# Performance work log

Measured on AMD Instinct MI355X. Metric: run time of the kernel, lower is better.

Reference implementation:

```python
import jax, jax.numpy as jnp
import numpy as np

B, C, H, W, S = 32, 512, 32, 32, 4
HW = H * W
OUT = HW // S  # conv1/conv2 out channels = 256
EPS = 1e-5


def setup_inputs() -> dict:
    key = jax.random.key(0)
    ks = jax.random.split(key, 8)
    d = {}
    d["x"] = jax.random.normal(ks[0], (B, C, H, W), jnp.float32)
    # conv1 / bn1 (operate on x_flat with 'channels' = h*w)
    d["w1"] = jax.random.normal(ks[1], (OUT, HW), jnp.float32) * 0.02
    d["b1"] = jnp.zeros((OUT,), jnp.float32)
    d["g1"] = jnp.ones((OUT,), jnp.float32)
    d["be1"] = jnp.zeros((OUT,), jnp.float32)
    d["m1"] = jax.random.normal(ks[2], (OUT,), jnp.float32) * 0.01
    d["v1"] = jnp.ones((OUT,), jnp.float32)
    # conv2 / bn2
    d["w2"] = jax.random.normal(ks[3], (OUT, HW), jnp.float32) * 0.02
    d["b2"] = jnp.zeros((OUT,), jnp.float32)
    d["g2"] = jnp.ones((OUT,), jnp.float32)
    d["be2"] = jnp.zeros((OUT,), jnp.float32)
    d["m2"] = jax.random.normal(ks[4], (OUT,), jnp.float32) * 0.01
    d["v2"] = jnp.ones((OUT,), jnp.float32)
    # conv3 / bn3 (1x1 conv on the real channel dim c)
    d["w3"] = jax.random.normal(ks[5], (C, C), jnp.float32) * 0.02
    d["b3"] = jnp.zeros((C,), jnp.float32)
    d["g3"] = jnp.ones((C,), jnp.float32)
    d["be3"] = jnp.zeros((C,), jnp.float32)
    d["m3"] = jax.random.normal(ks[6], (C,), jnp.float32) * 0.01
    d["v3"] = jnp.ones((C,), jnp.float32)
    # conv4: 1x1 conv mapping 1+2c channels -> 1
    d["w4"] = jax.random.normal(ks[7], (1 + 2 * C,), jnp.float32) * 0.02
    d["b4"] = jnp.zeros((), jnp.float32)
    return d


def _bn1d(t, g, be, m, v):
    # t: [b, o, c]; BatchNorm (eval mode) over channel axis 1
    scale = g / jnp.sqrt(v + EPS)
    return (t - m[:, None]) * scale[:, None] + be[:, None]


def reference(x, w1, b1, g1, be1, m1, v1,
              w2, b2, g2, be2, m2, v2,
              w3, b3, g3, be3, m3, v3,
              w4, b4):
    b, c, h, w = x.shape
    # x_flat: [b, h*w, c] -- conv1/conv2 are 1x1 convs over 'channels' = h*w
    xf = x.reshape(b, c, h * w).transpose(0, 2, 1)
    theta = jax.nn.relu(_bn1d(jnp.einsum('oq,bqc->boc', w1, xf) + b1[:, None],
                              g1, be1, m1, v1))  # [b, OUT, c]
    phi = jax.nn.relu(_bn1d(jnp.einsum('oq,bqc->boc', w2, xf) + b2[:, None],
                            g2, be2, m2, v2))    # [b, OUT, c]
    # per-batch conv2d-as-matmul loop collapses to one batched GEMM:
    # affinity[b, i, j] = sum_k phi[b, k, i] * theta[b, k, j]
    aff = jnp.einsum('bki,bkj->bij', phi, theta)  # [b, c, c]
    # x_embed: 1x1 conv + BN + ReLU + global average pool -> [b, c]
    scale3 = g3 / jnp.sqrt(v3 + EPS)
    xe = jnp.einsum('oc,bchw->bohw', w3, x) + b3[:, None, None]
    xe = jax.nn.relu((xe - m3[:, None, None]) * scale3[:, None, None]
                     + be3[:, None, None])
    xe = xe.mean(axis=(2, 3))  # [b, c]
    # conv4 over y = cat([x_embed, affinity_a, affinity_b], dim=1):
    # affinity_a[b,i,0,p] = aff[b,i,p]; affinity_b[b,i,0,p] = aff[b,p,i]
    logits = (w4[0] * xe
              + jnp.einsum('i,bip->bp', w4[1:1 + c], aff)
              + jnp.einsum('i,bpi->bp', w4[1 + c:], aff)
              + b4)
    a = jax.nn.sigmoid(logits)  # [b, c]
    return x * a[:, :, None, None]
```

## Files before the change

kernel.cpp:

```cpp
#include <hip/hip_runtime.h>
#include <math.h>

#define BB   32
#define CC   512
#define HWW  1024
#define OUTC 256
#define EPSV 1e-5f

typedef __attribute__((ext_vector_type(8))) short bfrag;
typedef __attribute__((ext_vector_type(4))) float f32x4;

__device__ inline unsigned short f2bf(float x){
  unsigned int uu = __float_as_uint(x);
  uu += 0x7fff + ((uu >> 16) & 1);
  return (unsigned short)(uu >> 16);
}
__device__ inline float bf2f(unsigned short h){
  return __uint_as_float(((unsigned int)h) << 16);
}

#define ASYNC16(g, l) \
  __builtin_amdgcn_global_load_lds((const __attribute__((address_space(1))) unsigned int*)(g), \
                                   (__attribute__((address_space(3))) unsigned int*)(l), 16, 0, 0)

#define WAITV(N) asm volatile("s_waitcnt vmcnt(" #N ")" ::: "memory")


__global__ __launch_bounds__(256) void prep(
    const float* __restrict__ x,
    const float* __restrict__ w1, const float* __restrict__ w2,
    const float* __restrict__ w3,
    unsigned short* __restrict__ Xhi, unsigned short* __restrict__ Xlo,
    unsigned short* __restrict__ XThi,
    unsigned short* __restrict__ Whi, unsigned short* __restrict__ Wlo,
    unsigned short* __restrict__ W3hi,
    float* __restrict__ accz)
{
  if (blockIdx.z == 32) {
    int worker = (blockIdx.y * 16 + blockIdx.x) * 256 + threadIdx.x;
    accz[worker] = 0.f;
    for (int i = worker; i < 786432; i += 32768) {
      if (i < 524288) {
        float v = (i < 262144) ? w1[i] : w2[i - 262144];
        unsigned short h = f2bf(v);
        Whi[i] = h;
        Wlo[i] = f2bf(v - bf2f(h));
      } else {
        int j = i - 524288;
        W3hi[j] = f2bf(w3[j]);
      }
    }
    return;
  }
  __shared__ float T[64][65];
  const int b = blockIdx.z, c0 = blockIdx.y * 64, p0 = blockIdx.x * 64;
  const int tid = threadIdx.x, tr = tid >> 4, tc4 = (tid & 15) * 4;
  const float* xb = x + (size_t)b * 512 * 1024;
#pragma unroll
  for (int r = 0; r < 4; ++r) {
    int c = c0 + tr + r * 16;
    float4 v = *(const float4*)(xb + (size_t)c * 1024 + p0 + tc4);
    T[tr + r * 16][tc4 + 0] = v.x; T[tr + r * 16][tc4 + 1] = v.y;
    T[tr + r * 16][tc4 + 2] = v.z; T[tr + r * 16][tc4 + 3] = v.w;
    ushort4 h, l;
    h.x = f2bf(v.x); l.x = f2bf(v.x - bf2f(h.x));
    h.y = f2bf(v.y); l.y = f2bf(v.y - bf2f(h.y));
    h.z = f2bf(v.z); l.z = f2bf(v.z - bf2f(h.z));
    h.w = f2bf(v.w); l.w = f2bf(v.w - bf2f(h.w));
    size_t idx = (size_t)b * 524288 + (size_t)c * 1024 + p0 + tc4;
    *(ushort4*)(Xhi + idx) = h;
    *(ushort4*)(Xlo + idx) = l;
  }
  __syncthreads();
#pragma unroll
  for (int r = 0; r < 4; ++r) {
    int pl = tr + r * 16;
    ushort4 h;
    h.x = f2bf(T[tc4 + 0][pl]); h.y = f2bf(T[tc4 + 1][pl]);
    h.z = f2bf(T[tc4 + 2][pl]); h.w = f2bf(T[tc4 + 3][pl]);
    *(ushort4*)(XThi + (size_t)b * 524288 + (size_t)(p0 + pl) * 512 + c0 + tc4) = h;
  }
}

__global__ __launch_bounds__(256) void gemm_fused(
    const unsigned short* __restrict__ Xhi, const unsigned short* __restrict__ Xlo,
    const unsigned short* __restrict__ Whi, const unsigned short* __restrict__ Wlo,
    const unsigned short* __restrict__ W3hi, const unsigned short* __restrict__ XThi,
    const float* __restrict__ b1p, const float* __restrict__ g1p,
    const float* __restrict__ be1p, const float* __restrict__ m1p, const float* __restrict__ v1p,
    const float* __restrict__ b2p, const float* __restrict__ g2p,
    const float* __restrict__ be2p, const float* __restrict__ m2p, const float* __restrict__ v2p,
    const float* __restrict__ b3p, const float* __restrict__ g3p,
    const float* __restrict__ be3p, const float* __restrict__ m3p, const float* __restrict__ v3p,
    const float* __restrict__ w4,
    float* __restrict__ P2, float* __restrict__ u, float* __restrict__ t,
    float* __restrict__ xe_acc)
{
  __shared__ unsigned short smem[24576];
  const int fid  = blockIdx.x;
  const int tid  = threadIdx.x;
  const int wave = tid >> 6, lane = tid & 63;
  const int lr = lane >> 2;
  const int lcs = ((lane & 3) ^ (lr & 3)) * 8;
  const int fr = lane & 15, fq = lane >> 4;
  const int fsw = (fq ^ (fr & 3)) * 8;

  if (fid < 1024) {
    const int xcd = fid & 7;
    const int n0  = ((fid >> 3) & 7) * 64;
    const int bc  = ((fid >> 6) << 3) | xcd;
    const int b   = bc >> 2;
    const int c0  = (bc & 3) * 128;
    const int wm = wave & 1, wn = wave >> 1;

    const unsigned short* gb; int lboff; int ninst;
    if (wave == 0)      { gb = Xhi + (size_t)b * 524288 + (size_t)c0 * 1024; lboff = 0;     ninst = 8; }
    else if (wave == 1) { gb = Xlo + (size_t)b * 524288 + (size_t)c0 * 1024; lboff = 4096;  ninst = 8; }
    else if (wave == 2) { gb = Whi + (size_t)n0 * 1024; lboff = 8192;  ninst = 4; }
    else                { gb = Wlo + (size_t)n0 * 1024; lboff = 10240; ninst = 4; }
    gb += (size_t)lr * 1024 + lcs;

    f32x4 acc[4][2];
    const f32x4 zz = {0.f, 0.f, 0.f, 0.f};
#pragma unroll
    for (int i = 0; i < 4; ++i) { acc[i][0] = zz; acc[i][1] = zz; }

    for (int inst = 0; inst < ninst; ++inst)
      ASYNC16(gb + (size_t)inst * 16 * 1024, smem + lboff + inst * 512);

    int cur = 0;
    for (int kq = 0; kq < 1024; kq += 32) {
      __builtin_amdgcn_sched_barrier(0);
      if (kq + 32 < 1024) {
        unsigned short* nb = smem + (cur ^ 1) * 12288 + lboff;
        for (int inst = 0; inst < ninst; ++inst)
          ASYNC16(gb + (size_t)inst * 16 * 1024 + kq + 32, nb + inst * 512);
        if (wave < 2) WAITV(8); else WAITV(4);
      } else {
        WAITV(0);
      }
      __builtin_amdgcn_s_barrier();
      __builtin_amdgcn_sched_barrier(0);

      const unsigned short* bufc = smem + cur * 12288;
      const unsigned short* sAh = bufc;
      const unsigned short* sAl = bufc + 4096;
      const unsigned short* sBh = bufc + 8192;
      const unsigned short* sBl = bufc + 10240;
      bfrag ah[4], al[4], bh[2], bl[2];
#pragma unroll
      for (int i = 0; i < 4; ++i) {
        int off = (wm * 64 + i * 16 + fr) * 32 + fsw;
        ah[i] = *(const bfrag*)&sAh[off];
        al[i] = *(const bfrag*)&sAl[off];
      }
#pragma unroll
      for (int j = 0; j < 2; ++j) {
        int off = (wn * 32 + j * 16 + fr) * 32 + fsw;
        bh[j] = *(const bfrag*)&sBh[off];
        bl[j] = *(const bfrag*)&sBl[off];
      }
#pragma unroll
      for (int i = 0; i < 4; ++i)
#pragma unroll
        for (int j = 0; j < 2; ++j) {
          acc[i][j] = __builtin_amdgcn_mfma_f32_16x16x32_bf16(ah[i], bh[j], acc[i][j], 0, 0, 0);
          acc[i][j] = __builtin_amdgcn_mfma_f32_16x16x32_bf16(ah[i], bl[j], acc[i][j], 0, 0, 0);
          acc[i][j] = __builtin_amdgcn_mfma_f32_16x16x32_bf16(al[i], bh[j], acc[i][j], 0, 0, 0);
        }
      __builtin_amdgcn_sched_barrier(0);
      __builtin_amdgcn_s_barrier();
      cur ^= 1;
    }
    __builtin_amdgcn_sched_barrier(0);

    const float *bias, *gg, *bes, *mm, *vv_; int cof;
    if (n0 < 256) { bias = b1p; gg = g1p; bes = be1p; mm = m1p; vv_ = v1p; cof = 0; }
    else          { bias = b2p; gg = g2p; bes = be2p; mm = m2p; vv_ = v2p; cof = 256; }
    const float* wsel = (n0 < 256) ? (w4 + 513) : (w4 + 1);
    float* dsel = (n0 < 256) ? (t + b * 256) : (u + b * 256);
    const int cobase = (n0 - cof) + wn * 32;
    float wt[4][4];
#pragma unroll
    for (int i = 0; i < 4; ++i)
#pragma unroll
      for (int r = 0; r < 4; ++r)
        wt[i][r] = wsel[c0 + wm * 64 + i * 16 + fq * 4 + r];

#pragma unroll
    for (int j = 0; j < 2; ++j) {
      int co = n0 + wn * 32 + j * 16 + fr;
      int q = co - cof;
      float s  = gg[q] * rsqrtf(vv_[q] + EPSV);
      float sh = (bias[q] - mm[q]) * s + bes[q];
      float psum = 0.f;
#pragma unroll
      for (int i = 0; i < 4; ++i) {
        int crow = c0 + wm * 64 + i * 16 + fq * 4;
        float* dst = P2 + ((size_t)b * 512 + crow) * 512 + co;
#pragma unroll
        for (int r = 0; r < 4; ++r) {
          float val = fmaxf(acc[i][j][r] * s + sh, 0.f);
          dst[(size_t)r * 512] = val;
          psum += wt[i][r] * val;
        }
      }
      psum += __shfl_xor(psum, 16);
      psum += __shfl_xor(psum, 32);
      if (fq == 0) atomicAdd(&dsel[cobase + j * 16 + fr], psum);
    }
  } else {
    const int h  = fid - 1024;
    const int n0 = (h & 7) * 128;
    const int m0 = ((h >> 3) & 3) * 128;
    const int b  = h >> 5;
    const int wm = wave & 1, wn = wave >> 1;

    const unsigned short* gb; int lboff;
    if (wave < 2) { gb = W3hi + (size_t)(m0 + wave * 64) * 512; lboff = wave * 2048; }
    else { gb = XThi + (size_t)b * 524288 + (size_t)(n0 + (wave - 2) * 64) * 512; lboff = 4096 + (wave - 2) * 2048; }
    gb += (size_t)lr * 512 + lcs;

    f32x4 acc[4][4];
    const f32x4 zz = {0.f, 0.f, 0.f, 0.f};
#pragma unroll
    for (int i = 0; i < 4; ++i)
#pragma unroll
      for (int j = 0; j < 4; ++j) acc[i][j] = zz;

#pragma unroll
    for (int inst = 0; inst < 4; ++inst)
      ASYNC16(gb + (size_t)inst * 16 * 512, smem + lboff + inst * 512);

    int cur = 0;
    for (int kq = 0; kq < 512; kq += 32) {
      __builtin_amdgcn_sched_barrier(0);
      if (kq + 32 < 512) {
        unsigned short* nb = smem + (cur ^ 1) * 8192 + lboff;
#pragma unroll
        for (int inst = 0; inst < 4; ++inst)
          ASYNC16(gb + (size_t)inst * 16 * 512 + kq + 32, nb + inst * 512);
        WAITV(4);
      } else {
        WAITV(0);
      }
      __builtin_amdgcn_s_barrier();
      __builtin_amdgcn_sched_barrier(0);

      const unsigned short* bufc = smem + cur * 8192;
      const unsigned short* sA = bufc;
      const unsigned short* sB = bufc + 4096;
      bfrag af[4], bf[4];
#pragma unroll
      for (int i = 0; i < 4; ++i)
        af[i] = *(const bfrag*)&sA[(wm * 64 + i * 16 + fr) * 32 + fsw];
#pragma unroll
      for (int j = 0; j < 4; ++j)
        bf[j] = *(const bfrag*)&sB[(wn * 64 + j * 16 + fr) * 32 + fsw];
#pragma unroll
      for (int i = 0; i < 4; ++i)
#pragma unroll
        for (int j = 0; j < 4; ++j)
          acc[i][j] = __builtin_amdgcn_mfma_f32_16x16x32_bf16(af[i], bf[j], acc[i][j], 0, 0, 0);
      __builtin_amdgcn_sched_barrier(0);
      __builtin_amdgcn_s_barrier();
      cur ^= 1;
    }
    __builtin_amdgcn_sched_barrier(0);

#pragma unroll
    for (int i = 0; i < 4; ++i) {
#pragma unroll
      for (int r = 0; r < 4; ++r) {
        int o = m0 + wm * 64 + i * 16 + fq * 4 + r;
        float s  = g3p[o] * rsqrtf(v3p[o] + EPSV);
        float sh = (b3p[o] - m3p[o]) * s + be3p[o];
        float v = fmaxf(acc[i][0][r] * s + sh, 0.f) + fmaxf(acc[i][1][r] * s + sh, 0.f)
                + fmaxf(acc[i][2][r] * s + sh, 0.f) + fmaxf(acc[i][3][r] * s + sh, 0.f);
        v += __shfl_xor(v, 1); v += __shfl_xor(v, 2);
        v += __shfl_xor(v, 4); v += __shfl_xor(v, 8);
        if (fr == 0) atomicAdd(&xe_acc[b * 512 + o], v);
      }
    }
  }
}

__global__ __launch_bounds__(256) void k4_gate_out(
    const float* __restrict__ P2, const float* __restrict__ u,
    const float* __restrict__ t, const float* __restrict__ xe_acc,
    const float* __restrict__ w4, const float* __restrict__ b4,
    const float* __restrict__ x, float* __restrict__ out)
{
  __shared__ float us[256], ts[256];
  const int b = blockIdx.x;
  us[threadIdx.x] = u[b * 256 + threadIdx.x];
  ts[threadIdx.x] = t[b * 256 + threadIdx.x];
  __syncthreads();
  const int wave = threadIdx.x >> 6, lane = threadIdx.x & 63;
  const int p = blockIdx.y * 4 + wave;
  const float* row = P2 + ((size_t)b * 512 + p) * 512;
  float4 th = *(const float4*)&row[lane * 4];
  float4 ph = *(const float4*)&row[256 + lane * 4];
  int ki = lane * 4;
  float rs = th.x * us[ki] + th.y * us[ki + 1] + th.z * us[ki + 2] + th.w * us[ki + 3]
           + ph.x * ts[ki] + ph.y * ts[ki + 1] + ph.z * ts[ki + 2] + ph.w * ts[ki + 3];
  rs += __shfl_xor(rs, 1);  rs += __shfl_xor(rs, 2);  rs += __shfl_xor(rs, 4);
  rs += __shfl_xor(rs, 8);  rs += __shfl_xor(rs, 16); rs += __shfl_xor(rs, 32);
  float xe = xe_acc[b * 512 + p] * (1.f / 1024.f);
  float logit = w4[0] * xe + rs + b4[0];
  float a = 1.f / (1.f + expf(-logit));
  const float4* xr = (const float4*)(x + ((size_t)b * 512 + p) * 1024);
  float4* orow = (float4*)(out + ((size_t)b * 512 + p) * 1024);
#pragma unroll
  for (int r2 = 0; r2 < 4; ++r2) {
    float4 xv = xr[lane + r2 * 64];
    float4 ov; ov.x = xv.x * a; ov.y = xv.y * a; ov.z = xv.z * a; ov.w = xv.w * a;
    orow[lane + r2 * 64] = ov;
  }
}

__global__ __launch_bounds__(256) void k1_theta_phi(
    const float* __restrict__ x,
    const float* __restrict__ w1, const float* __restrict__ b1,
    const float* __restrict__ g1, const float* __restrict__ be1,
    const float* __restrict__ m1, const float* __restrict__ v1,
    const float* __restrict__ w2, const float* __restrict__ b2,
    const float* __restrict__ g2, const float* __restrict__ be2,
    const float* __restrict__ m2, const float* __restrict__ v2,
    float* __restrict__ P)
{
  __shared__ __align__(16) float Ws[32][68];
  __shared__ __align__(16) float Xs[32][68];
  const int b  = blockIdx.z;
  const int o0 = blockIdx.y * 64;
  const int c0 = blockIdx.x * 64;
  const int tid = threadIdx.x;
  const int tx = tid & 15, ty = tid >> 4;
  const float* __restrict__ Wbase = (o0 < OUTC) ? (w1 + (size_t)o0 * HWW)
                                                : (w2 + (size_t)(o0 - OUTC) * HWW);
  const float* __restrict__ xb = x + (size_t)b * CC * HWW;
  float acc[4][4] = {{0.f}};
  for (int k0 = 0; k0 < HWW; k0 += 32) {
#pragma unroll
    for (int r = 0; r < 2; ++r) {
      int id  = tid + (r << 8);
      int row = id >> 3;
      int cg  = (id & 7) << 2;
      float4 wv = *(const float4*)(Wbase + (size_t)row * HWW + k0 + cg);
      Ws[cg+0][row] = wv.x; Ws[cg+1][row] = wv.y; Ws[cg+2][row] = wv.z; Ws[cg+3][row] = wv.w;
      float4 xv = *(const float4*)(xb + (size_t)(c0 + row) * HWW + k0 + cg);
      Xs[cg+0][row] = xv.x; Xs[cg+1][row] = xv.y; Xs[cg+2][row] = xv.z; Xs[cg+3][row] = xv.w;
    }
    __syncthreads();
#pragma unroll
    for (int k = 0; k < 32; ++k) {
      float4 av = *(const float4*)&Ws[k][ty * 4];
      float4 bv = *(const float4*)&Xs[k][tx * 4];
      acc[0][0] += av.x*bv.x; acc[0][1] += av.x*bv.y; acc[0][2] += av.x*bv.z; acc[0][3] += av.x*bv.w;
      acc[1][0] += av.y*bv.x; acc[1][1] += av.y*bv.y; acc[1][2] += av.y*bv.z; acc[1][3] += av.y*bv.w;
      acc[2][0] += av.z*bv.x; acc[2][1] += av.z*bv.y; acc[2][2] += av.z*bv.z; acc[2][3] += av.z*bv.w;
      acc[3][0] += av.w*bv.x; acc[3][1] += av.w*bv.y; acc[3][2] += av.w*bv.z; acc[3][3] += av.w*bv.w;
    }
    __syncthreads();
  }
  const float *bias, *g, *be, *m, *v; int ob;
  if (o0 < OUTC) { bias = b1; g = g1; be = be1; m = m1; v = v1; ob = o0; }
  else           { bias = b2; g = g2; be = be2; m = m2; v = v2; ob = o0 - OUTC; }
#pragma unroll
  for (int i = 0; i < 4; ++i) {
    int oi = ob + ty * 4 + i;
    float sc = g[oi] * rsqrtf(v[oi] + EPSV);
    float sh = be[oi] - m[oi] * sc;
    float bb = bias[oi];
    float4 ov;
    ov.x = fmaxf((acc[i][0] + bb) * sc + sh, 0.f);
    ov.y = fmaxf((acc[i][1] + bb) * sc + sh, 0.f);
    ov.z = fmaxf((acc[i][2] + bb) * sc + sh, 0.f);
    ov.w = fmaxf((acc[i][3] + bb) * sc + sh, 0.f);
    int oo = o0 + ty * 4 + i;
    *(float4*)(P + ((size_t)b * 512 + oo) * 512 + c0 + tx * 4) = ov;
  }
}

__global__ __launch_bounds__(256) void k2_xe(
    const float* __restrict__ x, const float* __restrict__ w3,
    const float* __restrict__ b3, const float* __restrict__ g3,
    const float* __restrict__ be3, const float* __restrict__ m3,
    const float* __restrict__ v3, float* __restrict__ xe_acc)
{
  __shared__ __align__(16) float As[32][68];
  __shared__ __align__(16) float Bs[32][68];
  const int b  = blockIdx.z;
  const int o0 = blockIdx.y * 64;
  const int p0 = blockIdx.x * 64;
  const int tid = threadIdx.x;
  const int tx = tid & 15, ty = tid >> 4;
  const float* __restrict__ xb = x + (size_t)b * CC * HWW;
  float acc[4][4] = {{0.f}};
  for (int ck = 0; ck < CC; ck += 32) {
#pragma unroll
    for (int r = 0; r < 2; ++r) {
      int id  = tid + (r << 8);
      int row = id >> 3;
      int cg  = (id & 7) << 2;
      float4 wv = *(const float4*)(w3 + (size_t)(o0 + row) * CC + ck + cg);
      As[cg+0][row] = wv.x; As[cg+1][row] = wv.y; As[cg+2][row] = wv.z; As[cg+3][row] = wv.w;
      int brow = id >> 4;
      int pg   = (id & 15) << 2;
      float4 xv = *(const float4*)(xb + (size_t)(ck + brow) * HWW + p0 + pg);
      *(float4*)&Bs[brow][pg] = xv;
    }
    __syncthreads();
#pragma unroll
    for (int k = 0; k < 32; ++k) {
      float4 av = *(const float4*)&As[k][ty * 4];
      float4 bv = *(const float4*)&Bs[k][tx * 4];
      acc[0][0] += av.x*bv.x; acc[0][1] += av.x*bv.y; acc[0][2] += av.x*bv.z; acc[0][3] += av.x*bv.w;
      acc[1][0] += av.y*bv.x; acc[1][1] += av.y*bv.y; acc[1][2] += av.y*bv.z; acc[1][3] += av.y*bv.w;
      acc[2][0] += av.z*bv.x; acc[2][1] += av.z*bv.y; acc[2][2] += av.z*bv.z; acc[2][3] += av.z*bv.w;
      acc[3][0] += av.w*bv.x; acc[3][1] += av.w*bv.y; acc[3][2] += av.w*bv.z; acc[3][3] += av.w*bv.w;
    }
    __syncthreads();
  }
#pragma unroll
  for (int i = 0; i < 4; ++i) {
    int oo = o0 + ty * 4 + i;
    float sc = g3[oo] * rsqrtf(v3[oo] + EPSV);
    float sh = be3[oo] - m3[oo] * sc;
    float bb = b3[oo];
    float ps = fmaxf((acc[i][0] + bb) * sc + sh, 0.f)
             + fmaxf((acc[i][1] + bb) * sc + sh, 0.f)
             + fmaxf((acc[i][2] + bb) * sc + sh, 0.f)
             + fmaxf((acc[i][3] + bb) * sc + sh, 0.f);
    ps += __shfl_xor(ps, 1);
    ps += __shfl_xor(ps, 2);
    ps += __shfl_xor(ps, 4);
    ps += __shfl_xor(ps, 8);
    if (tx == 0) atomicAdd(&xe_acc[b * CC + oo], ps);
  }
}

__global__ __launch_bounds__(256) void k3_ut(
    const float* __restrict__ P, const float* __restrict__ w4,
    float* __restrict__ u, float* __restrict__ t)
{
  const int b = blockIdx.x;
  const int wv = threadIdx.x >> 6, lane = threadIdx.x & 63;
  const int k = blockIdx.y * 4 + wv;
  const float* __restrict__ w4a = w4 + 1;
  const float* __restrict__ w4b = w4 + 1 + CC;
  const float* __restrict__ throw_ = P + ((size_t)b * 512 + k) * 512;
  const float* __restrict__ phrow  = P + ((size_t)b * 512 + 256 + k) * 512;
  float su = 0.f, st = 0.f;
#pragma unroll
  for (int i = lane; i < CC; i += 64) {
    su += w4a[i] * phrow[i];
    st += w4b[i] * throw_[i];
  }
#pragma unroll
  for (int off = 32; off > 0; off >>= 1) {
    su += __shfl_down(su, off);
    st += __shfl_down(st, off);
  }
  if (lane == 0) { u[b * OUTC + k] = su; t[b * OUTC + k] = st; }
}

__global__ __launch_bounds__(256) void k4_gate(
    const float* __restrict__ P, const float* __restrict__ u,
    const float* __restrict__ t, const float* __restrict__ xe_acc,
    const float* __restrict__ w4, const float* __restrict__ b4,
    float* __restrict__ amul)
{
  __shared__ float us[256], ts[256];
  const int b = blockIdx.x;
  const int p = blockIdx.y * 256 + threadIdx.x;
  us[threadIdx.x] = u[b * OUTC + threadIdx.x];
  ts[threadIdx.x] = t[b * OUTC + threadIdx.x];
  __syncthreads();
  const float* __restrict__ theta = P + (size_t)b * 512 * 512;
  const float* __restrict__ phi   = theta + 256 * 512;
  float r = 0.f, s = 0.f;
#pragma unroll 8
  for (int k = 0; k < OUTC; ++k) {
    r += us[k] * theta[(size_t)k * 512 + p];
    s += ts[k] * phi[(size_t)k * 512 + p];
  }
  float xe = xe_acc[b * CC + p] * (1.0f / 1024.0f);
  float logit = w4[0] * xe + r + s + b4[0];
  amul[b * CC + p] = 1.0f / (1.0f + expf(-logit));
}

__global__ __launch_bounds__(256) void k5_out(
    const float* __restrict__ x, const float* __restrict__ amul,
    float* __restrict__ out)
{
  int i = blockIdx.x * 256 + threadIdx.x;
  float4 xv = ((const float4*)x)[i];
  float a = amul[i >> 8];
  float4 ov; ov.x = xv.x * a; ov.y = xv.y * a; ov.z = xv.z * a; ov.w = xv.w * a;
  ((float4*)out)[i] = ov;
}

extern "C" void kernel_launch(void* const* d_in, const int* in_sizes, int n_in,
                              void* d_out, int out_size, void* d_ws, size_t ws_size,
                              hipStream_t stream)
{
  (void)in_sizes; (void)n_in; (void)out_size;
  const float* x   = (const float*)d_in[0];
  const float* w1  = (const float*)d_in[1];
  const float* b1  = (const float*)d_in[2];
  const float* g1  = (const float*)d_in[3];
  const float* be1 = (const float*)d_in[4];
  const float* m1  = (const float*)d_in[5];
  const float* v1  = (const float*)d_in[6];
  const float* w2  = (const float*)d_in[7];
  const float* b2  = (const float*)d_in[8];
  const float* g2  = (const float*)d_in[9];
  const float* be2 = (const float*)d_in[10];
  const float* m2  = (const float*)d_in[11];
  const float* v2  = (const float*)d_in[12];
  const float* w3  = (const float*)d_in[13];
  const float* b3  = (const float*)d_in[14];
  const float* g3  = (const float*)d_in[15];
  const float* be3 = (const float*)d_in[16];
  const float* m3  = (const float*)d_in[17];
  const float* v3  = (const float*)d_in[18];
  const float* w4  = (const float*)d_in[19];
  const float* b4  = (const float*)d_in[20];
  float* out = (float*)d_out;

  if (ws_size >= 136970240ull) {
    float* P2     = (float*)d_ws;
    float* xe_acc = P2 + 8388608;
    float* u      = P2 + 8404992;
    float* t      = P2 + 8413184;
    unsigned short* Xhi  = (unsigned short*)((char*)d_ws + 33685504);
    unsigned short* Xlo  = Xhi + 16777216;
    unsigned short* XThi = Xlo + 16777216;
    unsigned short* Whi  = XThi + 16777216;
    unsigned short* Wlo  = Whi + 524288;
    unsigned short* W3hi = Wlo + 524288;

    prep<<<dim3(16, 8, 33), 256, 0, stream>>>(x, w1, w2, w3, Xhi, Xlo, XThi,
                                              Whi, Wlo, W3hi, xe_acc);
    gemm_fused<<<dim3(2048), 256, 0, stream>>>(Xhi, Xlo, Whi, Wlo, W3hi, XThi,
        b1, g1, be1, m1, v1, b2, g2, be2, m2, v2, b3, g3, be3, m3, v3,
        w4, P2, u, t, xe_acc);
    k4_gate_out<<<dim3(32, 128), 256, 0, stream>>>(P2, u, t, xe_acc, w4, b4, x, out);
  } else {
    float* P      = (float*)d_ws;
    float* xe_acc = P + (size_t)BB * 512 * 512;
    float* u      = xe_acc + BB * CC;
    float* t      = u + BB * OUTC;
    float* amul   = t + BB * OUTC;

    hipMemsetAsync(xe_acc, 0, (size_t)BB * CC * sizeof(float), stream);

    dim3 blk(256);
    k1_theta_phi<<<dim3(8, 8, BB), blk, 0, stream>>>(x, w1, b1, g1, be1, m1, v1,
                                                     w2, b2, g2, be2, m2, v2, P);
    k2_xe<<<dim3(16, 8, BB), blk, 0, stream>>>(x, w3, b3, g3, be3, m3, v3, xe_acc);
    k3_ut<<<dim3(BB, 64), blk, 0, stream>>>(P, w4, u, t);
    k4_gate<<<dim3(BB, 2), blk, 0, stream>>>(P, u, t, xe_acc, w4, b4, amul);
    k5_out<<<dim3((BB * CC * HWW / 4) / 256), blk, 0, stream>>>(x, amul, out);
  }
}
```

Baseline: 287.1 us.

## Load weight GEMM operands directly from global into registers, shrink LDS

```diff
diff --git a/kernel.cpp b/kernel.cpp
--- a/kernel.cpp
+++ b/kernel.cpp
@@ -82,7 +82,7 @@
   }
 }
 
-__global__ __launch_bounds__(256) void gemm_fused(
+__global__ __launch_bounds__(256, 4) void gemm_fused(
     const unsigned short* __restrict__ Xhi, const unsigned short* __restrict__ Xlo,
     const unsigned short* __restrict__ Whi, const unsigned short* __restrict__ Wlo,
     const unsigned short* __restrict__ W3hi, const unsigned short* __restrict__ XThi,
@@ -96,7 +96,7 @@
     float* __restrict__ P2, float* __restrict__ u, float* __restrict__ t,
     float* __restrict__ xe_acc)
 {
-  __shared__ unsigned short smem[24576];
+  __shared__ unsigned short smem[16384];
   const int fid  = blockIdx.x;
   const int tid  = threadIdx.x;
   const int wave = tid >> 6, lane = tid & 63;
@@ -113,52 +113,53 @@
     const int c0  = (bc & 3) * 128;
     const int wm = wave & 1, wn = wave >> 1;
 
-    const unsigned short* gb; int lboff; int ninst;
-    if (wave == 0)      { gb = Xhi + (size_t)b * 524288 + (size_t)c0 * 1024; lboff = 0;     ninst = 8; }
-    else if (wave == 1) { gb = Xlo + (size_t)b * 524288 + (size_t)c0 * 1024; lboff = 4096;  ninst = 8; }
-    else if (wave == 2) { gb = Whi + (size_t)n0 * 1024; lboff = 8192;  ninst = 4; }
-    else                { gb = Wlo + (size_t)n0 * 1024; lboff = 10240; ninst = 4; }
-    gb += (size_t)lr * 1024 + lcs;
+    const unsigned short* gA = (wave < 2 ? Xhi : Xlo)
+        + (size_t)b * 524288 + (size_t)(c0 + (wave & 1) * 64) * 1024
+        + (size_t)lr * 1024 + lcs;
+    const int lA = ((wave < 2) ? 0 : 4096) + (wave & 1) * 2048;
+
+    const unsigned short* wbh = Whi + (size_t)(n0 + wn * 32 + fr) * 1024 + fq * 8;
+    const unsigned short* wbl = Wlo + (size_t)(n0 + wn * 32 + fr) * 1024 + fq * 8;
 
     f32x4 acc[4][2];
     const f32x4 zz = {0.f, 0.f, 0.f, 0.f};
 #pragma unroll
     for (int i = 0; i < 4; ++i) { acc[i][0] = zz; acc[i][1] = zz; }
 
-    for (int inst = 0; inst < ninst; ++inst)
-      ASYNC16(gb + (size_t)inst * 16 * 1024, smem + lboff + inst * 512);
+#pragma unroll
+    for (int inst = 0; inst < 4; ++inst)
+      ASYNC16(gA + (size_t)inst * 16 * 1024, smem + lA + inst * 512);
 
     int cur = 0;
     for (int kq = 0; kq < 1024; kq += 32) {
       __builtin_amdgcn_sched_barrier(0);
+      bfrag bh[2], bl[2];
+#pragma unroll
+      for (int j = 0; j < 2; ++j) {
+        bh[j] = *(const bfrag*)&wbh[j * 16384 + kq];
+        bl[j] = *(const bfrag*)&wbl[j * 16384 + kq];
+      }
+      __builtin_amdgcn_sched_barrier(0);
       if (kq + 32 < 1024) {
-        unsigned short* nb = smem + (cur ^ 1) * 12288 + lboff;
-        for (int inst = 0; inst < ninst; ++inst)
-          ASYNC16(gb + (size_t)inst * 16 * 1024 + kq + 32, nb + inst * 512);
-        if (wave < 2) WAITV(8); else WAITV(4);
+        unsigned short* nb = smem + (cur ^ 1) * 8192 + lA;
+#pragma unroll
+        for (int inst = 0; inst < 4; ++inst)
+          ASYNC16(gA + (size_t)inst * 16 * 1024 + kq + 32, nb + inst * 512);
+        WAITV(8);
       } else {
-        WAITV(0);
+        WAITV(4);
       }
       __builtin_amdgcn_s_barrier();
       __builtin_amdgcn_sched_barrier(0);
 
-      const unsigned short* bufc = smem + cur * 12288;
-      const unsigned short* sAh = bufc;
-      const unsigned short* sAl = bufc + 4096;
-      const unsigned short* sBh = bufc + 8192;
-      const unsigned short* sBl = bufc + 10240;
-      bfrag ah[4], al[4], bh[2], bl[2];
+      const unsigned short* sAh = smem + cur * 8192;
+      const unsigned short* sAl = sAh + 4096;
+      bfrag ah[4], al[4];
 #pragma unroll
       for (int i = 0; i < 4; ++i) {
         int off = (wm * 64 + i * 16 + fr) * 32 + fsw;
         ah[i] = *(const bfrag*)&sAh[off];
         al[i] = *(const bfrag*)&sAl[off];
-      }
-#pragma unroll
-      for (int j = 0; j < 2; ++j) {
-        int off = (wn * 32 + j * 16 + fr) * 32 + fsw;
-        bh[j] = *(const bfrag*)&sBh[off];
-        bl[j] = *(const bfrag*)&sBl[off];
       }
 #pragma unroll
       for (int i = 0; i < 4; ++i)
@@ -216,10 +217,11 @@
     const int b  = h >> 5;
     const int wm = wave & 1, wn = wave >> 1;
 
-    const unsigned short* gb; int lboff;
-    if (wave < 2) { gb = W3hi + (size_t)(m0 + wave * 64) * 512; lboff = wave * 2048; }
-    else { gb = XThi + (size_t)b * 524288 + (size_t)(n0 + (wave - 2) * 64) * 512; lboff = 4096 + (wave - 2) * 2048; }
-    gb += (size_t)lr * 512 + lcs;
+    const unsigned short* gB = XThi + (size_t)b * 524288
+        + (size_t)(n0 + wave * 32) * 512 + (size_t)lr * 512 + lcs;
+    const int lB = wave * 1024;
+
+    const unsigned short* wa = W3hi + (size_t)(m0 + wm * 64 + fr) * 512 + fq * 8;
 
     f32x4 acc[4][4];
     const f32x4 zz = {0.f, 0.f, 0.f, 0.f};
@@ -229,31 +231,31 @@
       for (int j = 0; j < 4; ++j) acc[i][j] = zz;
 
 #pragma unroll
-    for (int inst = 0; inst < 4; ++inst)
-      ASYNC16(gb + (size_t)inst * 16 * 512, smem + lboff + inst * 512);
+    for (int inst = 0; inst < 2; ++inst)
+      ASYNC16(gB + (size_t)inst * 16 * 512, smem + lB + inst * 512);
 
     int cur = 0;
     for (int kq = 0; kq < 512; kq += 32) {
       __builtin_amdgcn_sched_barrier(0);
+      bfrag af[4];
+#pragma unroll
+      for (int i = 0; i < 4; ++i)
+        af[i] = *(const bfrag*)&wa[i * 8192 + kq];
+      __builtin_amdgcn_sched_barrier(0);
       if (kq + 32 < 512) {
-        unsigned short* nb = smem + (cur ^ 1) * 8192 + lboff;
-#pragma unroll
-        for (int inst = 0; inst < 4; ++inst)
-          ASYNC16(gb + (size_t)inst * 16 * 512 + kq + 32, nb + inst * 512);
+        unsigned short* nb = smem + (cur ^ 1) * 4096 + lB;
+#pragma unroll
+        for (int inst = 0; inst < 2; ++inst)
+          ASYNC16(gB + (size_t)inst * 16 * 512 + kq + 32, nb + inst * 512);
+        WAITV(6);
+      } else {
         WAITV(4);
-      } else {
-        WAITV(0);
       }
       __builtin_amdgcn_s_barrier();
       __builtin_amdgcn_sched_barrier(0);
 
-      const unsigned short* bufc = smem + cur * 8192;
-      const unsigned short* sA = bufc;
-      const unsigned short* sB = bufc + 4096;
-      bfrag af[4], bf[4];
-#pragma unroll
-      for (int i = 0; i < 4; ++i)
-        af[i] = *(const bfrag*)&sA[(wm * 64 + i * 16 + fr) * 32 + fsw];
+      const unsigned short* sB = smem + cur * 4096;
+      bfrag bf[4];
 #pragma unroll
       for (int j = 0; j < 4; ++j)
         bf[j] = *(const bfrag*)&sB[(wn * 64 + j * 16 + fr) * 32 + fsw];
```

Result: slower. 317.4 us (+10.5%).
